# Kernel optimization log

Hardware: AMD Instinct MI355X
Metric: run time of the kernel (lower is better)

The kernel has to match this reference:

```python
import jax, jax.numpy as jnp
import numpy as np

B, S, D, C = 64, 576, 768, 200


def setup_inputs() -> dict:
    key = jax.random.key(0)
    k1, k2, k3, k4 = jax.random.split(key, 4)
    return {
        "patch_tokens": jax.random.normal(k1, (B, S, D), dtype=jnp.float32),
        "class_token": jax.random.normal(k2, (B, D), dtype=jnp.float32),
        "attn_w": jax.random.normal(k3, (C, D), dtype=jnp.float32) * (1.0 / np.sqrt(D)),
        "attn_b": jnp.zeros((C,), dtype=jnp.float32),
        "gc_w": jax.random.normal(k4, (C, D), dtype=jnp.float32) * (1.0 / np.sqrt(D)),
        "gc_b": jnp.zeros((C,), dtype=jnp.float32),
        "lam": jnp.ones((1,), dtype=jnp.float32),
    }


def reference(patch_tokens, class_token, attn_w, attn_b, gc_w, gc_b, lam):
    # patch_tokens: (B,S,D). The torch module reshapes S to HxW, but the mean
    # over (H,W) equals the mean over S, so we stay in token layout.
    _, S_, D_ = patch_tokens.shape
    # Global classifier: (B,C)
    global_scores = class_token @ gc_w.T + gc_b
    # Per-class 1x1 conv == per-class linear projection over tokens: (B,C,S)
    att = jax.nn.sigmoid(
        jnp.einsum("bsd,cd->bcs", patch_tokens, attn_w) + attn_b[None, :, None]
    )
    # mean over spatial (S) then mean over channels (D):
    # mean_d mean_s (att * feat) == einsum / (S*D)
    attention_scores = jnp.einsum("bcs,bsd->bc", att, patch_tokens) / (S_ * D_)
    return global_scores + lam[0] * attention_scores
```

## Files before the change

kernel.cpp:

```cpp
#include <hip/hip_runtime.h>
#include <math.h>

#define Bsz  64
#define Ssz  576
#define Dsz  768
#define Csz  200
#define NPAD 208
#define MT   32
#define BK   64
#define NKT  12

typedef short short8 __attribute__((ext_vector_type(8)));
typedef float f32x4  __attribute__((ext_vector_type(4)));

#define AS_GLOBAL __attribute__((address_space(1)))
#define AS_LDS    __attribute__((address_space(3)))

__device__ inline unsigned short f2bf_rne(float f) {
    union { float f; unsigned int u; } v; v.f = f;
    return (unsigned short)((v.u + 0x7FFFu + ((v.u >> 16) & 1u)) >> 16);
}
__device__ inline unsigned int pack2bf(float lo, float hi) {
    union { float f; unsigned int u; } a, b; a.f = lo; b.f = hi;
    return __builtin_amdgcn_perm(b.u + 0x8000u, a.u + 0x8000u, 0x07060302u);
}
__device__ inline void gload16(const unsigned short* g, unsigned short* l) {
    __builtin_amdgcn_global_load_lds((const AS_GLOBAL unsigned int*)g,
                                     (AS_LDS unsigned int*)l, 16, 0, 0);
}
__device__ inline void gload16f(const float* g, float* l) {
    __builtin_amdgcn_global_load_lds((const AS_GLOBAL unsigned int*)g,
                                     (AS_LDS unsigned int*)l, 16, 0, 0);
}

__global__ __launch_bounds__(256) void prep_w(const float* __restrict__ W,
                                              unsigned short* __restrict__ Wb) {
    const int i   = blockIdx.x * 256 + threadIdx.x;
    const int row = i / (Dsz / 4);
    const int col = (i % (Dsz / 4)) * 4;
    ushort4 h;
    if (row < Csz) {
        const float4 v = *(const float4*)(W + (size_t)row * Dsz + col);
        h.x = f2bf_rne(v.x); h.y = f2bf_rne(v.y); h.z = f2bf_rne(v.z); h.w = f2bf_rne(v.w);
    } else if (row == Csz) {
        h.x = h.y = h.z = h.w = 0x3F80;
    } else {
        h.x = h.y = h.z = h.w = 0;
    }
    *(ushort4*)(Wb + (size_t)row * Dsz + col) = h;
}

__global__ __launch_bounds__(256) void gc_kernel(
    const float* __restrict__ ct, const float* __restrict__ gw,
    const float* __restrict__ gb, float* __restrict__ out) {
    const int b    = blockIdx.x;
    const int wv   = threadIdx.x >> 6;
    const int lane = threadIdx.x & 63;
    const int c    = blockIdx.y * 4 + wv;
    const float* wr = gw + (size_t)c * Dsz + lane * 12;
    const float* cr = ct + (size_t)b * Dsz + lane * 12;
    float s = 0.f;
#pragma unroll
    for (int j = 0; j < 3; ++j) {
        const float4 w = *(const float4*)(wr + 4 * j);
        const float4 x = *(const float4*)(cr + 4 * j);
        s += w.x * x.x + w.y * x.y + w.z * x.z + w.w * x.w;
    }
#pragma unroll
    for (int off = 32; off > 0; off >>= 1) s += __shfl_down(s, off, 64);
    if (lane == 0) out[b * Csz + c] = s + gb[c];
}

__global__ __launch_bounds__(256, 4) void attn_kernel(
    const float* __restrict__ X,
    const unsigned short* __restrict__ Wb,
    const float* __restrict__ attn_b,
    const float* __restrict__ lam,
    float* __restrict__ out)
{
    __shared__ float sX[2][MT * BK];
    __shared__ unsigned short sW[2][NPAD * BK];
    __shared__ float rowsumL[MT];

    const int tid  = threadIdx.x;
    const int lane = tid & 63;
    const int w    = tid >> 6;
    const int g    = w >> 1;
    const int h    = w & 1;
    const int m    = lane & 15;
    const int q    = lane >> 4;
    const int NT   = h ? 6 : 7;
    const int t0   = h * 7;
    const int rowbase = blockIdx.x * MT;
    const int bidx    = rowbase / Ssz;

    const int sx0 = (w * 2) * 64 + lane;
    const int sx1 = sx0 + 64;
    const int xr0 = sx0 >> 4, xc0 = (sx0 & 15) ^ (xr0 & 15);
    const int xr1 = sx1 >> 4, xc1 = (sx1 & 15) ^ (xr1 & 15);
    const float* xg0 = X + (size_t)(rowbase + xr0) * Dsz + xc0 * 4;
    const float* xg1 = X + (size_t)(rowbase + xr1) * Dsz + xc1 * 4;

    const int wn   = (w < 2) ? 7 : 6;
    const int grp0 = (w < 2) ? w * 7 : 14 + (w - 2) * 6;
    const int s0    = grp0 * 64 + lane;
    const int wrow0 = s0 >> 3;
    const int wcg   = (s0 & 7) ^ (wrow0 & 7);
    const unsigned short* wg0 = Wb + (size_t)wrow0 * Dsz + wcg * 8;

    f32x4 acc[7];
#pragma unroll
    for (int t = 0; t < 7; ++t) acc[t] = (f32x4){0.f, 0.f, 0.f, 0.f};

    gload16f(xg0, &sX[0][(w * 2 + 0) * 256]);
    gload16f(xg1, &sX[0][(w * 2 + 1) * 256]);
#pragma unroll
    for (int j = 0; j < 7; ++j)
        if (j < wn) gload16(wg0 + (size_t)8 * j * Dsz, &sW[0][(grp0 + j) * 512]);

    const int rA  = g * 16 + m;
    const int rAx = rA & 15;

    for (int kt = 0; kt < NKT; ++kt) {
        const int p = kt & 1;
        __syncthreads();
        if (kt + 1 < NKT) {
            const int kk = (kt + 1) * BK;
            gload16f(xg0 + kk, &sX[p ^ 1][(w * 2 + 0) * 256]);
            gload16f(xg1 + kk, &sX[p ^ 1][(w * 2 + 1) * 256]);
#pragma unroll
            for (int j = 0; j < 7; ++j)
                if (j < wn) gload16(wg0 + (size_t)(kk + 8 * j * Dsz), &sW[p ^ 1][(grp0 + j) * 512]);
        }
#pragma unroll
        for (int k2 = 0; k2 < 2; ++k2) {
            const int cA = k2 * 8 + 2 * q;
            const float4 alo = *(const float4*)&sX[p][(rA * 16 + (cA ^ rAx)) * 4];
            const float4 ahi = *(const float4*)&sX[p][(rA * 16 + ((cA + 1) ^ rAx)) * 4];
            union { short8 s; unsigned int u[4]; } A;
            A.u[0] = pack2bf(alo.x, alo.y); A.u[1] = pack2bf(alo.z, alo.w);
            A.u[2] = pack2bf(ahi.x, ahi.y); A.u[3] = pack2bf(ahi.z, ahi.w);
            const unsigned short* wb = &sW[p][m * 64 + ((k2 * 4 + q) ^ (m & 7)) * 8];
#pragma unroll
            for (int t = 0; t < 7; ++t) {
                if (t < NT) {
                    const short8 bf = *(const short8*)(wb + (t0 + t) * 1024);
                    acc[t] = __builtin_amdgcn_mfma_f32_16x16x32_bf16(A.s, bf, acc[t], 0, 0, 0);
                }
            }
        }
    }

    if (h == 1 && m == 8) {
#pragma unroll
        for (int r = 0; r < 4; ++r) rowsumL[g * 16 + q * 4 + r] = acc[5][r];
    }
    __syncthreads();
    float rsv[4];
#pragma unroll
    for (int r = 0; r < 4; ++r) rsv[r] = rowsumL[g * 16 + q * 4 + r];

    const float scale = lam[0] * (1.f / ((float)Ssz * (float)Dsz));

#pragma unroll
    for (int t = 0; t < 7; ++t) {
        if (t < NT) {
            const int c = (t0 + t) * 16 + m;
            if (c < Csz) {
                const float bias = attn_b[c];
                float s = 0.f;
#pragma unroll
                for (int r = 0; r < 4; ++r)
                    s += rsv[r] / (1.f + __expf(-(acc[t][r] + bias)));
                s += __shfl_xor(s, 16, 64);
                s += __shfl_xor(s, 32, 64);
                if (q == 0) atomicAdd(&out[bidx * Csz + c], s * scale);
            }
        }
    }
}

extern "C" void kernel_launch(void* const* d_in, const int* in_sizes, int n_in,
                              void* d_out, int out_size, void* d_ws, size_t ws_size,
                              hipStream_t stream) {
    const float* X   = (const float*)d_in[0];
    const float* ct  = (const float*)d_in[1];
    const float* aw  = (const float*)d_in[2];
    const float* ab  = (const float*)d_in[3];
    const float* gw  = (const float*)d_in[4];
    const float* gb  = (const float*)d_in[5];
    const float* lam = (const float*)d_in[6];
    float* out = (float*)d_out;
    unsigned short* Wb = (unsigned short*)d_ws;

    prep_w<<<(NPAD * Dsz / 4) / 256, 256, 0, stream>>>(aw, Wb);
    gc_kernel<<<dim3(Bsz, Csz / 4), 256, 0, stream>>>(ct, gw, gb, out);
    attn_kernel<<<(Bsz * Ssz) / MT, 256, 0, stream>>>(X, Wb, ab, lam, out);
}
```

Baseline: 210.8 us.

## Use 64-row tiles with each wave computing all class tiles

Each block now covers 64 token rows instead of 32, with a 32-wide K step. Each wave owns 16 rows and computes all 13 class tiles, so the split of class tiles across wave pairs goes away. The block-wide row-sum exchange through shared memory and its extra barrier are replaced by a lane shuffle. Each loaded weight tile is reused across twice as many rows and A-fragment conversion is shared across all tiles. The cost is higher register pressure (13 accumulators, occupancy hint lowered to 3) and twice as many K iterations, each with its own barrier.

```diff
diff --git a/kernel.cpp b/kernel.cpp
--- a/kernel.cpp
+++ b/kernel.cpp
@@ -6,9 +6,9 @@
 #define Dsz  768
 #define Csz  200
 #define NPAD 208
-#define MT   32
-#define BK   64
-#define NKT  12
+#define MT   64
+#define BK   32
+#define NKT  24
 
 typedef short short8 __attribute__((ext_vector_type(8)));
 typedef float f32x4  __attribute__((ext_vector_type(4)));
@@ -71,7 +71,7 @@
     if (lane == 0) out[b * Csz + c] = s + gb[c];
 }
 
-__global__ __launch_bounds__(256, 4) void attn_kernel(
+__global__ __launch_bounds__(256, 3) void attn_kernel(
     const float* __restrict__ X,
     const unsigned short* __restrict__ Wb,
     const float* __restrict__ attn_b,
@@ -80,102 +80,83 @@
 {
     __shared__ float sX[2][MT * BK];
     __shared__ unsigned short sW[2][NPAD * BK];
-    __shared__ float rowsumL[MT];
 
     const int tid  = threadIdx.x;
     const int lane = tid & 63;
     const int w    = tid >> 6;
-    const int g    = w >> 1;
-    const int h    = w & 1;
     const int m    = lane & 15;
     const int q    = lane >> 4;
-    const int NT   = h ? 6 : 7;
-    const int t0   = h * 7;
     const int rowbase = blockIdx.x * MT;
     const int bidx    = rowbase / Ssz;
 
-    const int sx0 = (w * 2) * 64 + lane;
-    const int sx1 = sx0 + 64;
-    const int xr0 = sx0 >> 4, xc0 = (sx0 & 15) ^ (xr0 & 15);
-    const int xr1 = sx1 >> 4, xc1 = (sx1 & 15) ^ (xr1 & 15);
-    const float* xg0 = X + (size_t)(rowbase + xr0) * Dsz + xc0 * 4;
-    const float* xg1 = X + (size_t)(rowbase + xr1) * Dsz + xc1 * 4;
+    const int sxa  = w * 128 + lane;
+    const int xrow = sxa >> 3;
+    const int xgc  = (sxa & 7) ^ (xrow & 7);
+    const float* xg = X + (size_t)(rowbase + xrow) * Dsz + xgc * 4;
 
-    const int wn   = (w < 2) ? 7 : 6;
-    const int grp0 = (w < 2) ? w * 7 : 14 + (w - 2) * 6;
-    const int s0    = grp0 * 64 + lane;
-    const int wrow0 = s0 >> 3;
-    const int wcg   = (s0 & 7) ^ (wrow0 & 7);
-    const unsigned short* wg0 = Wb + (size_t)wrow0 * Dsz + wcg * 8;
+    const int wn    = (w < 3) ? 3 : 4;
+    const int grp0  = w * 3;
+    const int sw0   = grp0 * 64 + lane;
+    const int wrow0 = sw0 >> 2;
+    const int wgc   = (sw0 & 3) ^ (wrow0 & 3);
+    const unsigned short* wg = Wb + (size_t)wrow0 * Dsz + wgc * 8;
 
-    f32x4 acc[7];
+    const int rA    = w * 16 + m;
+    const int aoff0 = (rA * 8 + ((2 * q) ^ (rA & 7))) * 4;
+    const int aoff1 = (rA * 8 + ((2 * q + 1) ^ (rA & 7))) * 4;
+    const int boff  = (m * 4 + (q ^ (m & 3))) * 8;
+
+    f32x4 acc[13];
 #pragma unroll
-    for (int t = 0; t < 7; ++t) acc[t] = (f32x4){0.f, 0.f, 0.f, 0.f};
+    for (int t = 0; t < 13; ++t) acc[t] = (f32x4){0.f, 0.f, 0.f, 0.f};
 
-    gload16f(xg0, &sX[0][(w * 2 + 0) * 256]);
-    gload16f(xg1, &sX[0][(w * 2 + 1) * 256]);
+    gload16f(xg, &sX[0][w * 512]);
+    gload16f(xg + 8 * Dsz, &sX[0][w * 512 + 256]);
 #pragma unroll
-    for (int j = 0; j < 7; ++j)
-        if (j < wn) gload16(wg0 + (size_t)8 * j * Dsz, &sW[0][(grp0 + j) * 512]);
-
-    const int rA  = g * 16 + m;
-    const int rAx = rA & 15;
+    for (int j = 0; j < 4; ++j)
+        if (j < wn) gload16(wg + (size_t)16 * j * Dsz, &sW[0][(grp0 + j) * 512]);
 
     for (int kt = 0; kt < NKT; ++kt) {
         const int p = kt & 1;
         __syncthreads();
         if (kt + 1 < NKT) {
             const int kk = (kt + 1) * BK;
-            gload16f(xg0 + kk, &sX[p ^ 1][(w * 2 + 0) * 256]);
-            gload16f(xg1 + kk, &sX[p ^ 1][(w * 2 + 1) * 256]);
+            gload16f(xg + kk, &sX[p ^ 1][w * 512]);
+            gload16f(xg + kk + 8 * Dsz, &sX[p ^ 1][w * 512 + 256]);
 #pragma unroll
-            for (int j = 0; j < 7; ++j)
-                if (j < wn) gload16(wg0 + (size_t)(kk + 8 * j * Dsz), &sW[p ^ 1][(grp0 + j) * 512]);
+            for (int j = 0; j < 4; ++j)
+                if (j < wn) gload16(wg + (size_t)(kk + 16 * j * Dsz), &sW[p ^ 1][(grp0 + j) * 512]);
         }
+        const float4 alo = *(const float4*)&sX[p][aoff0];
+        const float4 ahi = *(const float4*)&sX[p][aoff1];
+        union { short8 s; unsigned int u[4]; } A;
+        A.u[0] = pack2bf(alo.x, alo.y); A.u[1] = pack2bf(alo.z, alo.w);
+        A.u[2] = pack2bf(ahi.x, ahi.y); A.u[3] = pack2bf(ahi.z, ahi.w);
 #pragma unroll
-        for (int k2 = 0; k2 < 2; ++k2) {
-            const int cA = k2 * 8 + 2 * q;
-            const float4 alo = *(const float4*)&sX[p][(rA * 16 + (cA ^ rAx)) * 4];
-            const float4 ahi = *(const float4*)&sX[p][(rA * 16 + ((cA + 1) ^ rAx)) * 4];
-            union { short8 s; unsigned int u[4]; } A;
-            A.u[0] = pack2bf(alo.x, alo.y); A.u[1] = pack2bf(alo.z, alo.w);
-            A.u[2] = pack2bf(ahi.x, ahi.y); A.u[3] = pack2bf(ahi.z, ahi.w);
-            const unsigned short* wb = &sW[p][m * 64 + ((k2 * 4 + q) ^ (m & 7)) * 8];
-#pragma unroll
-            for (int t = 0; t < 7; ++t) {
-                if (t < NT) {
-                    const short8 bf = *(const short8*)(wb + (t0 + t) * 1024);
-                    acc[t] = __builtin_amdgcn_mfma_f32_16x16x32_bf16(A.s, bf, acc[t], 0, 0, 0);
-                }
-            }
+        for (int t = 0; t < 13; ++t) {
+            const short8 bf = *(const short8*)&sW[p][boff + t * 512];
+            acc[t] = __builtin_amdgcn_mfma_f32_16x16x32_bf16(A.s, bf, acc[t], 0, 0, 0);
         }
     }
 
-    if (h == 1 && m == 8) {
-#pragma unroll
-        for (int r = 0; r < 4; ++r) rowsumL[g * 16 + q * 4 + r] = acc[5][r];
-    }
-    __syncthreads();
     float rsv[4];
 #pragma unroll
-    for (int r = 0; r < 4; ++r) rsv[r] = rowsumL[g * 16 + q * 4 + r];
+    for (int r = 0; r < 4; ++r) rsv[r] = __shfl(acc[12][r], (lane & 48) + 8, 64);
 
     const float scale = lam[0] * (1.f / ((float)Ssz * (float)Dsz));
 
 #pragma unroll
-    for (int t = 0; t < 7; ++t) {
-        if (t < NT) {
-            const int c = (t0 + t) * 16 + m;
-            if (c < Csz) {
-                const float bias = attn_b[c];
-                float s = 0.f;
+    for (int t = 0; t < 13; ++t) {
+        const int c = t * 16 + m;
+        if (c < Csz) {
+            const float bias = attn_b[c];
+            float s = 0.f;
 #pragma unroll
-                for (int r = 0; r < 4; ++r)
-                    s += rsv[r] / (1.f + __expf(-(acc[t][r] + bias)));
-                s += __shfl_xor(s, 16, 64);
-                s += __shfl_xor(s, 32, 64);
-                if (q == 0) atomicAdd(&out[bidx * Csz + c], s * scale);
-            }
+            for (int r = 0; r < 4; ++r)
+                s += rsv[r] / (1.f + __expf(-(acc[t][r] + bias)));
+            s += __shfl_xor(s, 16, 64);
+            s += __shfl_xor(s, 32, 64);
+            if (q == 0) atomicAdd(&out[bidx * Csz + c], s * scale);
         }
     }
 }
```

New measurement: 211.2 us. No clear change (+0.2%).
